# Kernel tuning notes

Measured on AMD Instinct MI355X. Metric: run time of the kernel, lower is better.

## Reference

```python
import jax, jax.numpy as jnp
import numpy as np

B, N, D, KD = 8, 2048, 64, 64

def setup_inputs() -> dict:
    key = jax.random.key(0)
    ks = jax.random.split(key, 7)
    s = 1.0 / np.sqrt(D)
    return {
        "x":  jax.random.normal(ks[0], (B, N, D), dtype=jnp.float32),
        "Wq": jax.random.normal(ks[1], (D, KD), dtype=jnp.float32) * s,
        "bq": jnp.zeros((KD,), jnp.float32),
        "Wk": jax.random.normal(ks[2], (D, KD), dtype=jnp.float32) * s,
        "bk": jnp.zeros((KD,), jnp.float32),
        "Wv": jax.random.normal(ks[3], (D, KD), dtype=jnp.float32) * s,
        "bv": jnp.zeros((KD,), jnp.float32),
    }

def reference(x, Wq, bq, Wk, bk, Wv, bv):
    # Q,K,V: [B,N,KD]
    Q = x @ Wq + bq
    K = x @ Wk + bk
    V = x @ Wv + bv
    # scores: [B,N,N] (note: original applies NO 1/sqrt(d) scaling)
    scores = jnp.einsum('bij,bkj->bik', Q, K)
    probs = jax.nn.softmax(scores, axis=-1)
    # mean-threshold sparsification: keep entries above the row mean
    mask = (probs > jnp.mean(probs, axis=-1, keepdims=True)).astype(probs.dtype)
    sparse = probs * mask
    out = jnp.einsum('bij,bjk->bik', sparse, V)  # [B,N,KD]
    return out
```

## Files before the change

kernel.cpp:

```cpp
#include <hip/hip_runtime.h>

#define NB 8
#define NS 2048
#define ND 64
#define LOG2E 1.44269504f
#define QSC 256.0f
#define IQS (1.0f / 256.0f)

#define KST 80
#define VST 136
#define KTILE (128 * KST)
#define VTILE (64 * VST)

typedef _Float16 half8 __attribute__((ext_vector_type(8)));
typedef _Float16 half4 __attribute__((ext_vector_type(4)));
typedef __attribute__((ext_vector_type(4))) float floatx4;
typedef unsigned uintx16 __attribute__((ext_vector_type(16)));

__device__ __forceinline__ half8 cvt8(const float* p) {
    float4 a = *(const float4*)p;
    float4 b = *(const float4*)(p + 4);
    half8 h = {(_Float16)a.x, (_Float16)a.y, (_Float16)a.z, (_Float16)a.w,
               (_Float16)b.x, (_Float16)b.y, (_Float16)b.z, (_Float16)b.w};
    return h;
}

__global__ __launch_bounds__(256) void wprep(
    const float* __restrict__ Wq, const float* __restrict__ Wk,
    const float* __restrict__ Wv, _Float16* __restrict__ Wt)
{
    const int m = blockIdx.x;
    const float* W = (m == 0) ? Wq : (m == 1) ? Wk : Wv;
    for (int i = threadIdx.x; i < 64 * 64; i += 256) {
        const int c = i >> 6, d = i & 63;
        Wt[((size_t)m * 64 + c) * 64 + d] = (_Float16)W[d * 64 + c];
    }
}

__global__ __launch_bounds__(256) void qkv_proj(
    const float* __restrict__ x, const _Float16* __restrict__ Wt,
    const float* __restrict__ bq, const float* __restrict__ bk,
    const float* __restrict__ bv,
    _Float16* __restrict__ Qg, _Float16* __restrict__ Kg,
    _Float16* __restrict__ Vt)
{
    __shared__ _Float16 vt[4][64 * 20];

    const int tid  = threadIdx.x;
    const int wv   = tid >> 6;
    const int l    = tid & 63;
    const int quad = l >> 4;
    const int tx   = l & 15;

    const int b  = blockIdx.x & 7;
    const int n0 = (blockIdx.x >> 3) * 64 + wv * 16;

    const float* xr = x + ((size_t)b * NS + n0 + tx) * ND + quad * 8;
    half8 a0 = cvt8(xr);
    half8 a1 = cvt8(xr + 32);

    const floatx4 zf = {0.f, 0.f, 0.f, 0.f};

#pragma unroll
    for (int ctile = 0; ctile < 12; ++ctile) {
        const int m    = ctile >> 2;
        const int lcol = (ctile & 3) * 16 + tx;

        const _Float16* Wb = Wt + ((size_t)m * 64 + lcol) * 64;
        half8 b0 = *(const half8*)(Wb + quad * 8);
        half8 b1 = *(const half8*)(Wb + 32 + quad * 8);

        floatx4 acc = __builtin_amdgcn_mfma_f32_16x16x32_f16(a0, b0, zf, 0, 0, 0);
        acc = __builtin_amdgcn_mfma_f32_16x16x32_f16(a1, b1, acc, 0, 0, 0);

        const float* Bp = (m == 0) ? bq : (m == 1) ? bk : bv;
        const float bias = Bp[lcol];

        if (m == 0) {
#pragma unroll
            for (int r = 0; r < 4; ++r)
                Qg[((size_t)b * NS + n0 + quad * 4 + r) * ND + lcol] =
                    (_Float16)((acc[r] + bias) * LOG2E);
        } else if (m == 1) {
#pragma unroll
            for (int r = 0; r < 4; ++r)
                Kg[((size_t)b * NS + n0 + quad * 4 + r) * ND + lcol] =
                    (_Float16)(acc[r] + bias);
        } else {
#pragma unroll
            for (int r = 0; r < 4; ++r)
                vt[wv][lcol * 20 + quad * 4 + r] = (_Float16)(acc[r] + bias);
        }
    }
    __syncthreads();
    {
        const int d = l;
        const _Float16* src = &vt[wv][d * 20];
        uint2 p0 = *(const uint2*)(src);
        uint2 p1 = *(const uint2*)(src + 4);
        uint2 p2 = *(const uint2*)(src + 8);
        uint2 p3 = *(const uint2*)(src + 12);
        uint4 q0 = {p0.x, p0.y, p1.x, p1.y};
        uint4 q1 = {p2.x, p2.y, p3.x, p3.y};
        _Float16* dst = Vt + ((size_t)b * ND + d) * NS + n0;
        *(uint4*)(dst)     = q0;
        *(uint4*)(dst + 8) = q1;
    }
}

__global__ __launch_bounds__(512, 4) void attn(
    const _Float16* __restrict__ Qg,
    const _Float16* __restrict__ Kg,
    const _Float16* __restrict__ Vt,
    float* __restrict__ out)
{
    __shared__ __align__(16) _Float16 smem[2 * KTILE];
    __shared__ float lsh[8 * 16];

    const int tid  = threadIdx.x;
    const int wv   = tid >> 6;
    const int l    = tid & 63;
    const int quad = l >> 4;
    const int tx   = l & 15;

    const int b  = blockIdx.x & 7;
    const int q0 = (blockIdx.x >> 3) * 16;

    const _Float16* Qb = Qg + ((size_t)b * NS + q0) * ND;
    const _Float16* Kb = Kg + (size_t)b * NS * ND;
    const _Float16* Vb = Vt + (size_t)b * ND * NS;

    half8 qf[2];
#pragma unroll
    for (int kc = 0; kc < 2; ++kc)
        qf[kc] = *(const half8*)(Qb + (size_t)tx * ND + kc * 32 + quad * 8);

    const floatx4 zf = {0.f, 0.f, 0.f, 0.f};

    uintx16 sx, sy;

    float lacc = 0.f;
    {
        const int skey = tid >> 2;
        const int sc0  = tid & 3;
        const _Float16* Ksrc = Kb + (size_t)skey * ND + sc0 * 8;
        const int kd = skey * KST + sc0 * 8;

        uint4 ga = *(const uint4*)Ksrc;
        uint4 gb = *(const uint4*)(Ksrc + 32);
        *(uint4*)(smem + kd) = ga;
        *(uint4*)(smem + kd + 32) = gb;

        const int krow = (wv * 16 + tx) * KST;

#pragma unroll
        for (int t = 0; t < 16; ++t) {
            const int buf = (t & 1) * KTILE;
            __syncthreads();
            if (t < 15) {
                ga = *(const uint4*)(Ksrc + (size_t)(t + 1) * 128 * ND);
                gb = *(const uint4*)(Ksrc + (size_t)(t + 1) * 128 * ND + 32);
            }
            half8 kf0 = *(const half8*)(smem + buf + krow + quad * 8);
            half8 kf1 = *(const half8*)(smem + buf + krow + 32 + quad * 8);
            floatx4 c = __builtin_amdgcn_mfma_f32_16x16x32_f16(kf0, qf[0], zf, 0, 0, 0);
            c = __builtin_amdgcn_mfma_f32_16x16x32_f16(kf1, qf[1], c, 0, 0, 0);
            int ic[4];
#pragma unroll
            for (int r = 0; r < 4; ++r) {
                float cs = fminf(fmaxf(c[r] * QSC, -32000.f), 32000.f);
                int v = (int)rintf(cs);
                ic[r] = v;
                lacc += __builtin_amdgcn_exp2f((float)v * IQS);
            }
            sx[t] = (unsigned)(ic[0] & 0xffff) | ((unsigned)ic[1] << 16);
            sy[t] = (unsigned)(ic[2] & 0xffff) | ((unsigned)ic[3] << 16);
            if (t < 15) {
                *(uint4*)(smem + (buf ^ KTILE) + kd) = ga;
                *(uint4*)(smem + (buf ^ KTILE) + kd + 32) = gb;
            }
        }
    }
#pragma unroll
    for (int off = 16; off < 64; off <<= 1)
        lacc += __shfl_xor(lacc, off);
    if (quad == 0)
        lsh[wv * 16 + tx] = lacc;

    const int sdim = tid >> 3;
    const int sv0  = tid & 7;
    const _Float16* Vsrc = Vb + (size_t)sdim * NS + sv0 * 8;
    const int vd = sdim * VST + sv0 * 8;

    uint4 gva = *(const uint4*)Vsrc;
    uint4 gvb = *(const uint4*)(Vsrc + 64);
    __syncthreads();

    float thr, inv;
    {
        float L = lsh[tx] + lsh[16 + tx] + lsh[32 + tx] + lsh[48 + tx]
                + lsh[64 + tx] + lsh[80 + tx] + lsh[96 + tx] + lsh[112 + tx];
        inv = 1.f / L;
        thr = L * (1.f / (float)NS);
    }

    *(uint4*)(smem + vd) = gva;
    *(uint4*)(smem + vd + 64) = gvb;

    floatx4 o[4] = {zf, zf, zf, zf};

#pragma unroll
    for (int t = 0; t < 16; ++t) {
        const int buf = (t & 1) * VTILE;
        __syncthreads();
        if (t < 15) {
            gva = *(const uint4*)(Vsrc + (size_t)(t + 1) * 128);
            gvb = *(const uint4*)(Vsrc + (size_t)(t + 1) * 128 + 64);
        }
        {
            const unsigned ux = sx[t], uy = sy[t];
            int s0 = (int)(short)(ux), s1 = (int)(short)(ux >> 16);
            int s2 = (int)(short)(uy), s3 = (int)(short)(uy >> 16);
            float e0 = __builtin_amdgcn_exp2f((float)s0 * IQS);
            float e1 = __builtin_amdgcn_exp2f((float)s1 * IQS);
            float e2 = __builtin_amdgcn_exp2f((float)s2 * IQS);
            float e3 = __builtin_amdgcn_exp2f((float)s3 * IQS);
            float w0 = (e0 > thr) ? e0 * inv : 0.f;
            float w1 = (e1 > thr) ? e1 * inv : 0.f;
            float w2 = (e2 > thr) ? e2 * inv : 0.f;
            float w3 = (e3 > thr) ? e3 * inv : 0.f;
            half4 af = {(_Float16)w0, (_Float16)w1, (_Float16)w2, (_Float16)w3};
#pragma unroll
            for (int dg = 0; dg < 4; ++dg) {
                half4 vf = *(const half4*)(smem + buf + (dg * 16 + tx) * VST +
                                           wv * 16 + quad * 4);
                o[dg] = __builtin_amdgcn_mfma_f32_16x16x16f16(af, vf, o[dg], 0, 0, 0);
            }
        }
        if (t < 15) {
            *(uint4*)(smem + (buf ^ VTILE) + vd) = gva;
            *(uint4*)(smem + (buf ^ VTILE) + vd + 64) = gvb;
        }
    }

    __syncthreads();
    float* osm = (float*)smem;
    const int orow = quad * 4;
    if (wv >= 4) {
        float* s = osm + (size_t)(wv - 4) * 16 * 68;
#pragma unroll
        for (int dg = 0; dg < 4; ++dg)
#pragma unroll
            for (int r = 0; r < 4; ++r)
                s[(orow + r) * 68 + dg * 16 + tx] = o[dg][r];
    }
    __syncthreads();
    if (wv < 4) {
        const float* s = osm + (size_t)wv * 16 * 68;
#pragma unroll
        for (int dg = 0; dg < 4; ++dg)
#pragma unroll
            for (int r = 0; r < 4; ++r)
                o[dg][r] += s[(orow + r) * 68 + dg * 16 + tx];
    }
    __syncthreads();
    if (wv == 2 || wv == 3) {
        float* s = osm + (size_t)(wv - 2) * 16 * 68;
#pragma unroll
        for (int dg = 0; dg < 4; ++dg)
#pragma unroll
            for (int r = 0; r < 4; ++r)
                s[(orow + r) * 68 + dg * 16 + tx] = o[dg][r];
    }
    __syncthreads();
    if (wv < 2) {
        const float* s = osm + (size_t)wv * 16 * 68;
#pragma unroll
        for (int dg = 0; dg < 4; ++dg)
#pragma unroll
            for (int r = 0; r < 4; ++r)
                o[dg][r] += s[(orow + r) * 68 + dg * 16 + tx];
    }
    __syncthreads();
    if (wv == 1) {
#pragma unroll
        for (int dg = 0; dg < 4; ++dg)
#pragma unroll
            for (int r = 0; r < 4; ++r)
                osm[(orow + r) * 68 + dg * 16 + tx] = o[dg][r];
    }
    __syncthreads();
    if (wv == 0) {
#pragma unroll
        for (int dg = 0; dg < 4; ++dg)
#pragma unroll
            for (int r = 0; r < 4; ++r)
                out[((size_t)b * NS + q0 + orow + r) * ND + dg * 16 + tx] =
                    o[dg][r] + osm[(orow + r) * 68 + dg * 16 + tx];
    }
}

extern "C" void kernel_launch(void* const* d_in, const int* in_sizes, int n_in,
                              void* d_out, int out_size, void* d_ws, size_t ws_size,
                              hipStream_t stream) {
    const float* x  = (const float*)d_in[0];
    const float* Wq = (const float*)d_in[1];
    const float* bq = (const float*)d_in[2];
    const float* Wk = (const float*)d_in[3];
    const float* bk = (const float*)d_in[4];
    const float* Wv = (const float*)d_in[5];
    const float* bv = (const float*)d_in[6];

    _Float16* Qg = (_Float16*)d_ws;
    _Float16* Kg = Qg + (size_t)NB * NS * ND;
    _Float16* Vt = Kg + (size_t)NB * NS * ND;
    _Float16* Wt = Vt + (size_t)NB * NS * ND;

    wprep<<<3, 256, 0, stream>>>(Wq, Wk, Wv, Wt);
    qkv_proj<<<NB * (NS / 64), 256, 0, stream>>>(x, Wt, bq, bk, bv, Qg, Kg, Vt);
    attn<<<NB * (NS / 16), 512, 0, stream>>>(Qg, Kg, Vt, (float*)d_out);
}
```

Baseline: 114.8 us.

## Load K straight to registers and stage V in per-wave LDS slabs

The block-wide double-buffered LDS staging of K is replaced by each wave loading its own 16-key fragments from global memory into registers, with a two-tile-ahead prefetch. V staging now uses a private LDS slab per wave, holding only the 16 keys that wave consumes. Both changes remove the per-iteration __syncthreads barriers in the score and PV loops. The trade-off is less coalesced global access patterns and extra register pressure from the prefetched fragments.

Result: slower. 150.4 us (+31.1%).

```diff
diff --git a/kernel.cpp b/kernel.cpp
--- a/kernel.cpp
+++ b/kernel.cpp
@@ -7,10 +7,8 @@
 #define QSC 256.0f
 #define IQS (1.0f / 256.0f)
 
-#define KST 80
-#define VST 136
-#define KTILE (128 * KST)
-#define VTILE (64 * VST)
+#define SST 20
+#define SLAB (64 * SST)
 
 typedef _Float16 half8 __attribute__((ext_vector_type(8)));
 typedef _Float16 half4 __attribute__((ext_vector_type(4)));
@@ -114,7 +112,7 @@
     const _Float16* __restrict__ Vt,
     float* __restrict__ out)
 {
-    __shared__ __align__(16) _Float16 smem[2 * KTILE];
+    __shared__ __align__(16) _Float16 smem[8 * SLAB];
     __shared__ float lsh[8 * 16];
 
     const int tid  = threadIdx.x;
@@ -141,30 +139,23 @@
 
     float lacc = 0.f;
     {
-        const int skey = tid >> 2;
-        const int sc0  = tid & 3;
-        const _Float16* Ksrc = Kb + (size_t)skey * ND + sc0 * 8;
-        const int kd = skey * KST + sc0 * 8;
-
-        uint4 ga = *(const uint4*)Ksrc;
-        uint4 gb = *(const uint4*)(Ksrc + 32);
-        *(uint4*)(smem + kd) = ga;
-        *(uint4*)(smem + kd + 32) = gb;
-
-        const int krow = (wv * 16 + tx) * KST;
+        const _Float16* Kw = Kb + (size_t)(wv * 16 + tx) * ND;
+        half8 ka[2], kc_[2];
+        ka[0]  = *(const half8*)(Kw + quad * 8);
+        kc_[0] = *(const half8*)(Kw + 32 + quad * 8);
+        ka[1]  = *(const half8*)(Kw + (size_t)128 * ND + quad * 8);
+        kc_[1] = *(const half8*)(Kw + (size_t)128 * ND + 32 + quad * 8);
 
 #pragma unroll
         for (int t = 0; t < 16; ++t) {
-            const int buf = (t & 1) * KTILE;
-            __syncthreads();
-            if (t < 15) {
-                ga = *(const uint4*)(Ksrc + (size_t)(t + 1) * 128 * ND);
-                gb = *(const uint4*)(Ksrc + (size_t)(t + 1) * 128 * ND + 32);
+            const int sl = t & 1;
+            half8 a0 = ka[sl], a1 = kc_[sl];
+            if (t < 14) {
+                ka[sl]  = *(const half8*)(Kw + (size_t)(t + 2) * 128 * ND + quad * 8);
+                kc_[sl] = *(const half8*)(Kw + (size_t)(t + 2) * 128 * ND + 32 + quad * 8);
             }
-            half8 kf0 = *(const half8*)(smem + buf + krow + quad * 8);
-            half8 kf1 = *(const half8*)(smem + buf + krow + 32 + quad * 8);
-            floatx4 c = __builtin_amdgcn_mfma_f32_16x16x32_f16(kf0, qf[0], zf, 0, 0, 0);
-            c = __builtin_amdgcn_mfma_f32_16x16x32_f16(kf1, qf[1], c, 0, 0, 0);
+            floatx4 c = __builtin_amdgcn_mfma_f32_16x16x32_f16(a0, qf[0], zf, 0, 0, 0);
+            c = __builtin_amdgcn_mfma_f32_16x16x32_f16(a1, qf[1], c, 0, 0, 0);
             int ic[4];
 #pragma unroll
             for (int r = 0; r < 4; ++r) {
@@ -175,10 +166,6 @@
             }
             sx[t] = (unsigned)(ic[0] & 0xffff) | ((unsigned)ic[1] << 16);
             sy[t] = (unsigned)(ic[2] & 0xffff) | ((unsigned)ic[3] << 16);
-            if (t < 15) {
-                *(uint4*)(smem + (buf ^ KTILE) + kd) = ga;
-                *(uint4*)(smem + (buf ^ KTILE) + kd + 32) = gb;
-            }
         }
     }
 #pragma unroll
@@ -187,13 +174,11 @@
     if (quad == 0)
         lsh[wv * 16 + tx] = lacc;
 
-    const int sdim = tid >> 3;
-    const int sv0  = tid & 7;
-    const _Float16* Vsrc = Vb + (size_t)sdim * NS + sv0 * 8;
-    const int vd = sdim * VST + sv0 * 8;
-
-    uint4 gva = *(const uint4*)Vsrc;
-    uint4 gvb = *(const uint4*)(Vsrc + 64);
+    _Float16* slab = smem + wv * SLAB;
+    const _Float16* Vw = Vb + (size_t)l * NS + wv * 16;
+    uint4 gva = *(const uint4*)Vw;
+    uint4 gvb = *(const uint4*)(Vw + 8);
+
     __syncthreads();
 
     float thr, inv;
@@ -204,20 +189,22 @@
         thr = L * (1.f / (float)NS);
     }
 
-    *(uint4*)(smem + vd) = gva;
-    *(uint4*)(smem + vd + 64) = gvb;
-
     floatx4 o[4] = {zf, zf, zf, zf};
 
-#pragma unroll
-    for (int t = 0; t < 16; ++t) {
-        const int buf = (t & 1) * VTILE;
-        __syncthreads();
-        if (t < 15) {
-            gva = *(const uint4*)(Vsrc + (size_t)(t + 1) * 128);
-            gvb = *(const uint4*)(Vsrc + (size_t)(t + 1) * 128 + 64);
-        }
-        {
+    {
+        _Float16* wrow = slab + l * SST;
+#pragma unroll
+        for (int t = 0; t < 16; ++t) {
+            uint2 w0 = {gva.x, gva.y}, w1 = {gva.z, gva.w};
+            uint2 w2 = {gvb.x, gvb.y}, w3 = {gvb.z, gvb.w};
+            *(uint2*)(wrow)      = w0;
+            *(uint2*)(wrow + 4)  = w1;
+            *(uint2*)(wrow + 8)  = w2;
+            *(uint2*)(wrow + 12) = w3;
+            if (t < 15) {
+                gva = *(const uint4*)(Vw + (size_t)(t + 1) * 128);
+                gvb = *(const uint4*)(Vw + (size_t)(t + 1) * 128 + 8);
+            }
             const unsigned ux = sx[t], uy = sy[t];
             int s0 = (int)(short)(ux), s1 = (int)(short)(ux >> 16);
             int s2 = (int)(short)(uy), s3 = (int)(short)(uy >> 16);
@@ -225,21 +212,16 @@
             float e1 = __builtin_amdgcn_exp2f((float)s1 * IQS);
             float e2 = __builtin_amdgcn_exp2f((float)s2 * IQS);
             float e3 = __builtin_amdgcn_exp2f((float)s3 * IQS);
-            float w0 = (e0 > thr) ? e0 * inv : 0.f;
-            float w1 = (e1 > thr) ? e1 * inv : 0.f;
-            float w2 = (e2 > thr) ? e2 * inv : 0.f;
-            float w3 = (e3 > thr) ? e3 * inv : 0.f;
-            half4 af = {(_Float16)w0, (_Float16)w1, (_Float16)w2, (_Float16)w3};
+            float w0f = (e0 > thr) ? e0 * inv : 0.f;
+            float w1f = (e1 > thr) ? e1 * inv : 0.f;
+            float w2f = (e2 > thr) ? e2 * inv : 0.f;
+            float w3f = (e3 > thr) ? e3 * inv : 0.f;
+            half4 af = {(_Float16)w0f, (_Float16)w1f, (_Float16)w2f, (_Float16)w3f};
 #pragma unroll
             for (int dg = 0; dg < 4; ++dg) {
-                half4 vf = *(const half4*)(smem + buf + (dg * 16 + tx) * VST +
-                                           wv * 16 + quad * 4);
+                half4 vf = *(const half4*)(slab + (dg * 16 + tx) * SST + quad * 4);
                 o[dg] = __builtin_amdgcn_mfma_f32_16x16x16f16(af, vf, o[dg], 0, 0, 0);
             }
-        }
-        if (t < 15) {
-            *(uint4*)(smem + (buf ^ VTILE) + vd) = gva;
-            *(uint4*)(smem + (buf ^ VTILE) + vd + 64) = gvb;
         }
     }
 
```
